# Kernel optimization log

Measured on AMD Instinct MI355X. Metric: run time of the kernel, lower is better.

The kernel has to match this reference:

```python
import jax, jax.numpy as jnp
import numpy as np

D_MODEL, N_HEADS, D_FF = 768, 12, 3072
B, S = 2, 2048
EPS = 1e-6

def _ln(x, alpha, bias):
    # Matches torch: std with Bessel correction (unbiased), scalar alpha/bias
    mean = x.mean(axis=-1, keepdims=True)
    std = jnp.std(x, axis=-1, keepdims=True, ddof=1)
    return alpha * (x - mean) / (std + EPS) + bias

def setup_inputs() -> dict:
    key = jax.random.key(0)
    ks = jax.random.split(key, 12)
    def w(k, shp):
        return jax.random.normal(k, shp, dtype=jnp.float32) * 0.02
    inp = {
        "x": jax.random.normal(ks[0], (B, S, D_MODEL), dtype=jnp.float32),
        "mask": jnp.ones((B, 1, 1, S), dtype=jnp.int32),
        "wq": w(ks[1], (D_MODEL, D_MODEL)), "bq": jnp.zeros((D_MODEL,), jnp.float32),
        "wk": w(ks[2], (D_MODEL, D_MODEL)), "bk": jnp.zeros((D_MODEL,), jnp.float32),
        "wv": w(ks[3], (D_MODEL, D_MODEL)), "bv": jnp.zeros((D_MODEL,), jnp.float32),
        "wo": w(ks[4], (D_MODEL, D_MODEL)), "bo": jnp.zeros((D_MODEL,), jnp.float32),
        "w1": w(ks[5], (D_MODEL, D_FF)), "b1": jnp.zeros((D_FF,), jnp.float32),
        "w2": w(ks[6], (D_FF, D_MODEL)), "b2": jnp.zeros((D_MODEL,), jnp.float32),
        "ln1_a": jnp.ones((1,), jnp.float32), "ln1_b": jnp.zeros((1,), jnp.float32),
        "ln2_a": jnp.ones((1,), jnp.float32), "ln2_b": jnp.zeros((1,), jnp.float32),
    }
    return inp

def reference(x, mask, wq, bq, wk, bk, wv, bv, wo, bo, w1, b1, w2, b2,
              ln1_a, ln1_b, ln2_a, ln2_b):
    d_k = D_MODEL // N_HEADS
    # --- residual 1: pre-LN self-attention ---
    h = _ln(x, ln1_a, ln1_b)
    q = (h @ wq + bq).reshape(B, S, N_HEADS, d_k).transpose(0, 2, 1, 3)
    k = (h @ wk + bk).reshape(B, S, N_HEADS, d_k).transpose(0, 2, 1, 3)
    v = (h @ wv + bv).reshape(B, S, N_HEADS, d_k).transpose(0, 2, 1, 3)
    scores = jnp.einsum('bhqd,bhkd->bhqk', q, k) / jnp.sqrt(jnp.float32(d_k))
    scores = jnp.where(mask == 0, jnp.float32(-1e9), scores)
    attn = jax.nn.softmax(scores, axis=-1)            # [B,H,S,S] materialized, as in source
    ctx = jnp.einsum('bhqk,bhkd->bhqd', attn, v)
    ctx = ctx.transpose(0, 2, 1, 3).reshape(B, S, D_MODEL)
    x = x + (ctx @ wo + bo)
    # --- residual 2: pre-LN FFN ---
    h = _ln(x, ln2_a, ln2_b)
    ffn = jax.nn.relu(h @ w1 + b1) @ w2 + b2
    return x + ffn
```

## Files before the change

kernel.cpp:

```cpp
#include <hip/hip_runtime.h>
#include <math.h>

#define DM    768
#define NH    12
#define DKH   64
#define DFF   3072
#define BATCH 2
#define SLEN  2048
#define MTOT  4096
#define LNEPS 1e-6f
#define QSCALE 0.18033688011112042f

typedef unsigned short u16;
typedef __attribute__((ext_vector_type(8))) short bf16x8;
typedef __attribute__((ext_vector_type(4))) float f32x4;
typedef __attribute__((ext_vector_type(4))) unsigned short us4;

__device__ __forceinline__ u16 f2bf(float f) {
    union { float f; unsigned int u; } v; v.f = f;
    unsigned int r = v.u + 0x7FFFu + ((v.u >> 16) & 1u);
    return (u16)(r >> 16);
}

__device__ __forceinline__ unsigned pk2bf_t(float lo, float hi) {
    union { float f; unsigned u; } a, b;
    a.f = lo; b.f = hi;
    return __builtin_amdgcn_perm(b.u, a.u, 0x07060302u);
}

__device__ __forceinline__ void gld16(const void* g, void* lds) {
    __builtin_amdgcn_global_load_lds(
        (const __attribute__((address_space(1))) unsigned int*)(unsigned long long)g,
        (__attribute__((address_space(3))) unsigned int*)(unsigned int)(unsigned long long)lds,
        16, 0, 0);
}

__device__ __forceinline__ void xcd_map(int id, int Nb, int& bm, int& bn) {
    int xcd = id & 7, loc = id >> 3;
    bn = loc % Nb;
    bm = (loc / Nb) * 8 + xcd;
}

__device__ __forceinline__ void ln_body(const float* __restrict__ x,
                                        u16* __restrict__ out,
                                        const float* __restrict__ alpha_p,
                                        const float* __restrict__ beta_p,
                                        const float* __restrict__ b2,
                                        float* __restrict__ out2, int row) {
    const float* xr = x + (size_t)row * DM;
    int t = threadIdx.x;
    float v0 = xr[t], v1 = xr[t + 256], v2 = xr[t + 512];
    float s = v0 + v1 + v2;
    #pragma unroll
    for (int off = 32; off > 0; off >>= 1) s += __shfl_down(s, off);
    __shared__ float red[4], red2[4];
    int wv = t >> 6, ln = t & 63;
    if (ln == 0) red[wv] = s;
    __syncthreads();
    float mean = (red[0] + red[1] + red[2] + red[3]) * (1.0f / 768.0f);
    float d0 = v0 - mean, d1 = v1 - mean, d2 = v2 - mean;
    float sq = d0 * d0 + d1 * d1 + d2 * d2;
    #pragma unroll
    for (int off = 32; off > 0; off >>= 1) sq += __shfl_down(sq, off);
    if (ln == 0) red2[wv] = sq;
    __syncthreads();
    float var = (red2[0] + red2[1] + red2[2] + red2[3]) * (1.0f / 767.0f);
    float scale = alpha_p[0] / (sqrtf(var) + LNEPS);
    float bias = beta_p[0];
    u16* orow = out + (size_t)row * DM;
    orow[t]       = f2bf(d0 * scale + bias);
    orow[t + 256] = f2bf(d1 * scale + bias);
    orow[t + 512] = f2bf(d2 * scale + bias);
    if (out2) {
        float* o2 = out2 + (size_t)row * DM;
        o2[t]       = v0 + b2[t];
        o2[t + 256] = v1 + b2[t + 256];
        o2[t + 512] = v2 + b2[t + 512];
    }
}

__global__ __launch_bounds__(256) void ln_kernel(const float* __restrict__ x,
                                                 u16* __restrict__ out,
                                                 const float* __restrict__ alpha_p,
                                                 const float* __restrict__ beta_p,
                                                 const float* __restrict__ b2,
                                                 float* __restrict__ out2) {
    ln_body(x, out, alpha_p, beta_p, b2, out2, blockIdx.x);
}

__device__ __forceinline__ void wcast_body(const float* __restrict__ src,
                                           u16* __restrict__ dst,
                                           int R, int C, int bx, int by) {
    __shared__ float tile[32][33];
    int t = threadIdx.x, tx = t & 31, ty = t >> 5;
    int r0 = by * 32, c0 = bx * 32;
    #pragma unroll
    for (int p = 0; p < 4; p++)
        tile[ty + p * 8][tx] = src[(size_t)(r0 + ty + p * 8) * C + c0 + tx];
    __syncthreads();
    #pragma unroll
    for (int p = 0; p < 4; p++)
        dst[(size_t)(c0 + ty + p * 8) * R + r0 + tx] = f2bf(tile[tx][ty + p * 8]);
}

__global__ __launch_bounds__(256) void prep_kernel(
        const float* __restrict__ x, u16* __restrict__ h,
        const float* __restrict__ ln1a, const float* __restrict__ ln1b,
        const float* __restrict__ wq, const float* __restrict__ wk,
        const float* __restrict__ wv, const float* __restrict__ wo,
        const float* __restrict__ w1, const float* __restrict__ w2,
        u16* __restrict__ wqT, u16* __restrict__ wkT, u16* __restrict__ wvT,
        u16* __restrict__ woT, u16* __restrict__ w1T, u16* __restrict__ w2T) {
    int bid = blockIdx.x;
    if (bid < MTOT) {
        ln_body(x, h, ln1a, ln1b, nullptr, nullptr, bid);
        return;
    }
    bid -= MTOT;
    const float* src; u16* dst; int R, C, bx, by;
    if (bid < 2304) {
        int j = bid / 576, tix = bid % 576;
        R = 768; C = 768; bx = tix % 24; by = tix / 24;
        src = (j == 0) ? wq : (j == 1) ? wk : (j == 2) ? wv : wo;
        dst = (j == 0) ? wqT : (j == 1) ? wkT : (j == 2) ? wvT : woT;
    } else if (bid < 4608) {
        int tix = bid - 2304;
        R = 768; C = 3072; bx = tix % 96; by = tix / 96;
        src = w1; dst = w1T;
    } else {
        int tix = bid - 4608;
        R = 3072; C = 768; bx = tix % 24; by = tix / 24;
        src = w2; dst = w2T;
    }
    wcast_body(src, dst, R, C, bx, by);
}

template<int EPI>
__device__ __forceinline__ void gemm128_core(const u16* __restrict__ A,
                                             const u16* __restrict__ Wt,
                                             const float* __restrict__ bias,
                                             const float* __restrict__ resid,
                                             void* __restrict__ Cout,
                                             int M, int N, int Kstride, int Kloop,
                                             float scale, int bm, int bn) {
    __shared__ __align__(16) u16 As[2][128 * 32];
    __shared__ __align__(16) u16 Bs[2][128 * 32];
    int t = threadIdx.x;
    int ln = t & 63, w = t >> 6;
    int wm = w >> 1, wn = w & 1;
    int quad = ln >> 4, col = ln & 15;
    int m0 = bm * 128, n0 = bn * 128;

    f32x4 acc[4][4];
    const f32x4 zero = {0.f, 0.f, 0.f, 0.f};
    #pragma unroll
    for (int i = 0; i < 4; i++)
        #pragma unroll
        for (int j = 0; j < 4; j++) acc[i][j] = zero;

    int st_ch = (((ln & 3) ^ ((ln >> 3) & 3))) * 8;
    const u16* Ag = A  + (size_t)(m0 + 32 * w + (ln >> 2)) * Kstride + st_ch;
    const u16* Bg = Wt + (size_t)(n0 + 32 * w + (ln >> 2)) * Kstride + st_ch;

    gld16(Ag,                As[0] + w * 1024);
    gld16(Ag + 16 * Kstride, As[0] + w * 1024 + 512);
    gld16(Bg,                Bs[0] + w * 1024);
    gld16(Bg + 16 * Kstride, Bs[0] + w * 1024 + 512);
    __syncthreads();

    int rch = (quad ^ ((col >> 1) & 3)) * 8;

    for (int k0 = 0; k0 < Kloop; k0 += 32) {
        int cur = (k0 >> 5) & 1, nxt = cur ^ 1;
        if (k0 + 32 < Kloop) {
            gld16(Ag + k0 + 32,                As[nxt] + w * 1024);
            gld16(Ag + k0 + 32 + 16 * Kstride, As[nxt] + w * 1024 + 512);
            gld16(Bg + k0 + 32,                Bs[nxt] + w * 1024);
            gld16(Bg + k0 + 32 + 16 * Kstride, Bs[nxt] + w * 1024 + 512);
        }
        bf16x8 af[4], bfr[4];
        #pragma unroll
        for (int i = 0; i < 4; i++)
            af[i] = *(const bf16x8*)&As[cur][(wm * 64 + i * 16 + col) * 32 + rch];
        #pragma unroll
        for (int j = 0; j < 4; j++)
            bfr[j] = *(const bf16x8*)&Bs[cur][(wn * 64 + j * 16 + col) * 32 + rch];
        #pragma unroll
        for (int i = 0; i < 4; i++)
            #pragma unroll
            for (int j = 0; j < 4; j++)
                acc[i][j] = __builtin_amdgcn_mfma_f32_16x16x32_bf16(af[i], bfr[j], acc[i][j], 0, 0, 0);
        __syncthreads();
    }

    #pragma unroll
    for (int i = 0; i < 4; i++) {
        int mb = m0 + wm * 64 + i * 16 + quad * 4;
        #pragma unroll
        for (int j = 0; j < 4; j++) {
            int n = n0 + wn * 64 + j * 16 + col;
            if (EPI == 0 || EPI == 1) {
                float bs = bias[n];
                u16* Cb = (u16*)Cout;
                #pragma unroll
                for (int r = 0; r < 4; r++) {
                    float f = (acc[i][j][r] + bs) * ((EPI == 0) ? scale : 1.0f);
                    if (EPI == 1) f = fmaxf(f, 0.f);
                    Cb[(size_t)(mb + r) * N + n] = f2bf(f);
                }
            } else if (EPI == 2) {
                float bs = bias[n];
                float* Cf = (float*)Cout;
                #pragma unroll
                for (int r = 0; r < 4; r++)
                    Cf[(size_t)(mb + r) * N + n] =
                        acc[i][j][r] + bs + resid[(size_t)(mb + r) * N + n];
            } else if (EPI == 3) {
                float bs = bias[n];
                u16* Cb = (u16*)Cout;
                us4 pk;
                #pragma unroll
                for (int r = 0; r < 4; r++) pk[r] = f2bf(acc[i][j][r] + bs);
                *(us4*)&Cb[(size_t)n * M + mb] = pk;
            } else {
                float* Cf = (float*)Cout;
                #pragma unroll
                for (int r = 0; r < 4; r++)
                    atomicAdd(&Cf[(size_t)(mb + r) * N + n], acc[i][j][r]);
            }
        }
    }
}

template<int EPI>
__global__ __launch_bounds__(256) void gemm_kernel(const u16* __restrict__ A,
                                                   const u16* __restrict__ Wt,
                                                   const float* __restrict__ bias,
                                                   const float* __restrict__ resid,
                                                   void* __restrict__ C,
                                                   int M, int N, int Kstride, int Kloop,
                                                   float scale, int Nb) {
    const u16* Az = A  + (size_t)blockIdx.z * Kloop;
    const u16* Wz = Wt + (size_t)blockIdx.z * Kloop;
    int bm, bn;
    xcd_map(blockIdx.x, Nb, bm, bn);
    gemm128_core<EPI>(Az, Wz, bias, resid, C, M, N, Kstride, Kloop, scale, bm, bn);
}

__global__ __launch_bounds__(256) void qkv_kernel(const u16* __restrict__ h,
        const u16* __restrict__ wqT, const u16* __restrict__ wkT, const u16* __restrict__ wvT,
        const float* __restrict__ bq, const float* __restrict__ bk, const float* __restrict__ bv,
        u16* __restrict__ q, u16* __restrict__ k, u16* __restrict__ vT) {
    int z = blockIdx.z;
    int bm, bn;
    xcd_map(blockIdx.x, 6, bm, bn);
    if (z == 0)      gemm128_core<0>(h, wqT, bq, nullptr, q,  MTOT, DM, DM, DM, QSCALE, bm, bn);
    else if (z == 1) gemm128_core<0>(h, wkT, bk, nullptr, k,  MTOT, DM, DM, DM, 1.0f,   bm, bn);
    else             gemm128_core<3>(h, wvT, bv, nullptr, vT, MTOT, DM, DM, DM, 1.0f,   bm, bn);
}

template<int EPI>
__global__ __launch_bounds__(256) void gemm64_kernel(const u16* __restrict__ A,
                                                     const u16* __restrict__ Wt,
                                                     const float* __restrict__ bias,
                                                     const float* __restrict__ resid,
                                                     void* __restrict__ Cout,
                                                     int M, int N, int Kstride, int Kloop,
                                                     int Nb) {
    __shared__ __align__(16) u16 As[2][64 * 32];
    __shared__ __align__(16) u16 Bs[2][64 * 32];
    int t = threadIdx.x, ln = t & 63, w = t >> 6;
    int wm = w >> 1, wn = w & 1;
    int quad = ln >> 4, col = ln & 15;
    int bm, bn;
    xcd_map(blockIdx.x, Nb, bm, bn);
    int m0 = bm * 64, n0 = bn * 64;

    f32x4 acc[2][2];
    const f32x4 zero = {0.f, 0.f, 0.f, 0.f};
    #pragma unroll
    for (int i = 0; i < 2; i++)
        #pragma unroll
        for (int j = 0; j < 2; j++) acc[i][j] = zero;

    int st_ch = (((ln & 3) ^ ((ln >> 3) & 3))) * 8;
    const u16* Ag = A  + (size_t)(m0 + 16 * w + (ln >> 2)) * Kstride + st_ch;
    const u16* Bg = Wt + (size_t)(n0 + 16 * w + (ln >> 2)) * Kstride + st_ch;
    gld16(Ag, As[0] + w * 512);
    gld16(Bg, Bs[0] + w * 512);
    __syncthreads();

    int rch = (quad ^ ((col >> 1) & 3)) * 8;

    for (int k0 = 0; k0 < Kloop; k0 += 32) {
        int cur = (k0 >> 5) & 1, nxt = cur ^ 1;
        if (k0 + 32 < Kloop) {
            gld16(Ag + k0 + 32, As[nxt] + w * 512);
            gld16(Bg + k0 + 32, Bs[nxt] + w * 512);
        }
        bf16x8 af[2], bfr[2];
        #pragma unroll
        for (int i = 0; i < 2; i++)
            af[i] = *(const bf16x8*)&As[cur][(wm * 32 + i * 16 + col) * 32 + rch];
        #pragma unroll
        for (int j = 0; j < 2; j++)
            bfr[j] = *(const bf16x8*)&Bs[cur][(wn * 32 + j * 16 + col) * 32 + rch];
        #pragma unroll
        for (int i = 0; i < 2; i++)
            #pragma unroll
            for (int j = 0; j < 2; j++)
                acc[i][j] = __builtin_amdgcn_mfma_f32_16x16x32_bf16(af[i], bfr[j], acc[i][j], 0, 0, 0);
        __syncthreads();
    }

    #pragma unroll
    for (int i = 0; i < 2; i++) {
        int mb = m0 + wm * 32 + i * 16 + quad * 4;
        #pragma unroll
        for (int j = 0; j < 2; j++) {
            int n = n0 + wn * 32 + j * 16 + col;
            float bs = bias[n];
            float* Cf = (float*)Cout;
            #pragma unroll
            for (int r = 0; r < 4; r++)
                Cf[(size_t)(mb + r) * N + n] =
                    acc[i][j][r] + bs + resid[(size_t)(mb + r) * N + n];
        }
    }
}

__global__ __launch_bounds__(256) void attn_kernel(const u16* __restrict__ qg,
                                                   const u16* __restrict__ kg,
                                                   const u16* __restrict__ vTg,
                                                   const int* __restrict__ mask,
                                                   u16* __restrict__ ctx) {
    __shared__ __align__(16) u16 Qs[64 * 64];
    __shared__ __align__(16) u16 KV[4][64 * 64];
    __shared__ __align__(16) u16 Ps[4][32 * 40];
    __shared__ __align__(16) float Msf[2][64];
    __shared__ float Lp[64];
    int t = threadIdx.x, ln = t & 63, w = t >> 6;
    int quad = ln >> 4, col = ln & 15;
    int qh = w >> 1, kh = w & 1;
    int bh = blockIdx.x, qb = blockIdx.y;
    int b = bh / NH, h = bh - b * NH;
    int q0 = qb * 64;
    size_t qkbase = ((size_t)b * SLEN) * DM + h * DKH;
    size_t vbase  = ((size_t)h * DKH) * MTOT + (size_t)b * SLEN;

    int sw_st = (((ln & 7) ^ (ln >> 3)) * 8);

    {
        const u16* g0 = qg + qkbase + (size_t)(q0 + 16 * w + (ln >> 3)) * DM + sw_st;
        gld16(g0,          Qs + w * 1024);
        gld16(g0 + 8 * DM, Qs + w * 1024 + 512);
        const u16* kg0 = kg + qkbase + (size_t)(16 * w + (ln >> 3)) * DM + sw_st;
        gld16(kg0,          KV[0] + w * 1024);
        gld16(kg0 + 8 * DM, KV[0] + w * 1024 + 512);
        const u16* vg0 = vTg + vbase + (size_t)(16 * w + (ln >> 3)) * MTOT + sw_st;
        gld16(vg0,            KV[2] + w * 1024);
        gld16(vg0 + 8 * MTOT, KV[2] + w * 1024 + 512);
        if (t < 64) Msf[0][t] = mask[b * SLEN + t] ? 0.f : -1e9f;
    }
    __syncthreads();

    bf16x8 bqf[2][2];
    #pragma unroll
    for (int qgi = 0; qgi < 2; qgi++) {
        int rq = qh * 32 + qgi * 16 + col;
        int cq = ((quad ^ (rq & 7)) * 8);
        bqf[qgi][0] = *(const bf16x8*)&Qs[rq * 64 + cq];
        bqf[qgi][1] = *(const bf16x8*)&Qs[rq * 64 + (cq ^ 32)];
    }

    bf16x8 vones;
    #pragma unroll
    for (int i = 0; i < 8; i++) vones[i] = (short)0x3F80;

    const u16* kpn = kg + qkbase + (size_t)(64 + 16 * w + (ln >> 3)) * DM + sw_st;
    const u16* vpn = vTg + vbase + (size_t)(16 * w + (ln >> 3)) * MTOT + 64 + sw_st;
    const int* mpn = mask + b * SLEN + 64 + t;

    f32x4 Ov[2][4], Lv[2];
    const f32x4 zero = {0.f, 0.f, 0.f, 0.f};
    #pragma unroll
    for (int qgi = 0; qgi < 2; qgi++) {
        Lv[qgi] = zero;
        #pragma unroll
        for (int dg = 0; dg < 4; dg++) Ov[qgi][dg] = zero;
    }
    u16* Psw = &Ps[w][0];

    for (int j0 = 0; j0 < SLEN; j0 += 64) {
        int cur = (j0 >> 6) & 1, nxt = cur ^ 1;
        if (j0 + 64 < SLEN) {
            gld16(kpn,            KV[nxt] + w * 1024);
            gld16(kpn + 8 * DM,   KV[nxt] + w * 1024 + 512);
            gld16(vpn,            KV[2 + nxt] + w * 1024);
            gld16(vpn + 8 * MTOT, KV[2 + nxt] + w * 1024 + 512);
            if (t < 64) Msf[nxt][t] = *mpn ? 0.f : -1e9f;
            kpn += 64 * DM; vpn += 64; mpn += 64;
        }

        bf16x8 ak[2][2];
        #pragma unroll
        for (int kgi = 0; kgi < 2; kgi++) {
            int rk = kh * 32 + kgi * 16 + col;
            int ck = ((quad ^ (rk & 7)) * 8);
            ak[kgi][0] = *(const bf16x8*)&KV[cur][rk * 64 + ck];
            ak[kgi][1] = *(const bf16x8*)&KV[cur][rk * 64 + (ck ^ 32)];
        }
        #pragma unroll
        for (int kgi = 0; kgi < 2; kgi++) {
            f32x4 bias4 = *(const f32x4*)&Msf[cur][kh * 32 + kgi * 16 + quad * 4];
            #pragma unroll
            for (int qgi = 0; qgi < 2; qgi++) {
                f32x4 S = __builtin_amdgcn_mfma_f32_16x16x32_bf16(ak[kgi][0], bqf[qgi][0], bias4, 0, 0, 0);
                S       = __builtin_amdgcn_mfma_f32_16x16x32_bf16(ak[kgi][1], bqf[qgi][1], S,     0, 0, 0);
                float p0 = exp2f(S[0]), p1 = exp2f(S[1]);
                float p2 = exp2f(S[2]), p3 = exp2f(S[3]);
                uint2 pk;
                pk.x = pk2bf_t(p0, p1);
                pk.y = pk2bf_t(p2, p3);
                *(uint2*)&Psw[(qgi * 16 + col) * 40 + kgi * 16 + quad * 4] = pk;
            }
        }
        bf16x8 ap[2];
        #pragma unroll
        for (int qgi = 0; qgi < 2; qgi++) {
            ap[qgi] = *(const bf16x8*)&Psw[(qgi * 16 + col) * 40 + quad * 8];
            Lv[qgi] = __builtin_amdgcn_mfma_f32_16x16x32_bf16(ap[qgi], vones, Lv[qgi], 0, 0, 0);
        }
        #pragma unroll
        for (int dg = 0; dg < 4; dg++) {
            int rv = dg * 16 + col;
            int cv = (((kh * 4 + quad) ^ (rv & 7)) * 8);
            bf16x8 bv = *(const bf16x8*)&KV[2 + cur][rv * 64 + cv];
            Ov[0][dg] = __builtin_amdgcn_mfma_f32_16x16x32_bf16(ap[0], bv, Ov[0][dg], 0, 0, 0);
            Ov[1][dg] = __builtin_amdgcn_mfma_f32_16x16x32_bf16(ap[1], bv, Ov[1][dg], 0, 0, 0);
        }
        __syncthreads();
    }

    float* Osh = (float*)&KV[0][0];
    if (kh == 1) {
        #pragma unroll
        for (int qgi = 0; qgi < 2; qgi++) {
            #pragma unroll
            for (int dg = 0; dg < 4; dg++)
                *(f32x4*)&Osh[(qh * 64 + dg * 16 + col) * 36 + qgi * 16 + quad * 4] = Ov[qgi][dg];
            if (col == 0) {
                #pragma unroll
                for (int r = 0; r < 4; r++)
                    Lp[qh * 32 + qgi * 16 + quad * 4 + r] = Lv[qgi][r];
            }
        }
    }
    __syncthreads();
    if (kh == 0) {
        #pragma unroll
        for (int qgi = 0; qgi < 2; qgi++) {
            float linv[4];
            #pragma unroll
            for (int r = 0; r < 4; r++) {
                int ql = qh * 32 + qgi * 16 + quad * 4 + r;
                linv[r] = 1.0f / (Lv[qgi][r] + Lp[ql]);
            }
            #pragma unroll
            for (int dg = 0; dg < 4; dg++) {
                f32x4 oo = *(const f32x4*)&Osh[(qh * 64 + dg * 16 + col) * 36 + qgi * 16 + quad * 4];
                #pragma unroll
                for (int r = 0; r < 4; r++) {
                    int qrow = q0 + qh * 32 + qgi * 16 + quad * 4 + r;
                    ctx[qkbase + (size_t)qrow * DM + dg * 16 + col] =
                        f2bf((Ov[qgi][dg][r] + oo[r]) * linv[r]);
                }
            }
        }
    }
}

extern "C" void kernel_launch(void* const* d_in, const int* in_sizes, int n_in,
                              void* d_out, int out_size, void* d_ws, size_t ws_size,
                              hipStream_t stream) {
    const float* x    = (const float*)d_in[0];
    const int*   mask = (const int*)d_in[1];
    const float* wq   = (const float*)d_in[2];
    const float* bq   = (const float*)d_in[3];
    const float* wk   = (const float*)d_in[4];
    const float* bk   = (const float*)d_in[5];
    const float* wv   = (const float*)d_in[6];
    const float* bv   = (const float*)d_in[7];
    const float* wo   = (const float*)d_in[8];
    const float* bo   = (const float*)d_in[9];
    const float* w1   = (const float*)d_in[10];
    const float* b1   = (const float*)d_in[11];
    const float* w2   = (const float*)d_in[12];
    const float* b2   = (const float*)d_in[13];
    const float* ln1a = (const float*)d_in[14];
    const float* ln1b = (const float*)d_in[15];
    const float* ln2a = (const float*)d_in[16];
    const float* ln2b = (const float*)d_in[17];
    float* out = (float*)d_out;

    char* w8 = (char*)d_ws;
    u16*   ffn = (u16*)(w8 + 0);
    u16*   q   = (u16*)(w8 + 0);
    u16*   kb  = (u16*)(w8 + 6291456);
    u16*   vT  = (u16*)(w8 + 12582912);
    u16*   ctx = (u16*)(w8 + 18874368);
    u16*   h   = (u16*)(w8 + 25165824);
    float* x1  = (float*)(w8 + 31457280);
    u16*   wqT = (u16*)(w8 + 44040192);
    u16*   wkT = (u16*)(w8 + 45219840);
    u16*   wvT = (u16*)(w8 + 46399488);
    u16*   woT = (u16*)(w8 + 47579136);
    u16*   w1T = (u16*)(w8 + 48758784);
    u16*   w2T = (u16*)(w8 + 53477376);

    prep_kernel<<<MTOT + 6912, 256, 0, stream>>>(x, h, ln1a, ln1b,
                                                 wq, wk, wv, wo, w1, w2,
                                                 wqT, wkT, wvT, woT, w1T, w2T);
    qkv_kernel<<<dim3(192, 1, 3), 256, 0, stream>>>(h, wqT, wkT, wvT, bq, bk, bv, q, kb, vT);
    attn_kernel<<<dim3(BATCH * NH, SLEN / 64), 256, 0, stream>>>(q, kb, vT, mask, ctx);
    gemm64_kernel<2><<<768, 256, 0, stream>>>(ctx, woT, bo, x, (void*)x1,
                                              MTOT, DM, DM, DM, 12);
    ln_kernel<<<MTOT, 256, 0, stream>>>(x1, h, ln2a, ln2b, b2, out);
    gemm_kernel<1><<<768, 256, 0, stream>>>(h, w1T, b1, nullptr, (void*)ffn,
                                            MTOT, DFF, DM, DM, 1.0f, 24);
    gemm_kernel<5><<<dim3(192, 1, 2), 256, 0, stream>>>(ffn, w2T, nullptr, nullptr, (void*)out,
                                                        MTOT, DM, DFF, DFF / 2, 1.0f, 6);
}
```

Before: 285.7 us.

## Keep softmax probabilities in registers for PV MFMA, drop LDS round-trip

The attention kernel used to write exp'd scores to a per-wave LDS buffer and read them back as MFMA A operands. Now it feeds the probabilities straight from registers into 16x16x16 bf16 MFMAs, computing the transposed output O^T = V^T P^T and the row sums with a ones vector. This removes LDS stores and loads and the buffer itself. The epilogue is also restructured to normalize in LDS and then write ctx with vectorized bf16 stores, with an extra barrier. The trade-off is twice as many MFMA instructions at half the K depth, plus one more sync in the epilogue.

```diff
diff --git a/kernel.cpp b/kernel.cpp
--- a/kernel.cpp
+++ b/kernel.cpp
@@ -13,6 +13,7 @@
 
 typedef unsigned short u16;
 typedef __attribute__((ext_vector_type(8))) short bf16x8;
+typedef __attribute__((ext_vector_type(4))) short bf16x4;
 typedef __attribute__((ext_vector_type(4))) float f32x4;
 typedef __attribute__((ext_vector_type(4))) unsigned short us4;
 
@@ -336,7 +337,6 @@
                                                    u16* __restrict__ ctx) {
     __shared__ __align__(16) u16 Qs[64 * 64];
     __shared__ __align__(16) u16 KV[4][64 * 64];
-    __shared__ __align__(16) u16 Ps[4][32 * 40];
     __shared__ __align__(16) float Msf[2][64];
     __shared__ float Lp[64];
     int t = threadIdx.x, ln = t & 63, w = t >> 6;
@@ -373,23 +373,22 @@
         bqf[qgi][1] = *(const bf16x8*)&Qs[rq * 64 + (cq ^ 32)];
     }
 
-    bf16x8 vones;
-    #pragma unroll
-    for (int i = 0; i < 8; i++) vones[i] = (short)0x3F80;
+    bf16x4 aones;
+    #pragma unroll
+    for (int i = 0; i < 4; i++) aones[i] = (short)0x3F80;
 
     const u16* kpn = kg + qkbase + (size_t)(64 + 16 * w + (ln >> 3)) * DM + sw_st;
     const u16* vpn = vTg + vbase + (size_t)(16 * w + (ln >> 3)) * MTOT + 64 + sw_st;
     const int* mpn = mask + b * SLEN + 64 + t;
 
-    f32x4 Ov[2][4], Lv[2];
+    f32x4 Ot[2][4], Lv[2];
     const f32x4 zero = {0.f, 0.f, 0.f, 0.f};
     #pragma unroll
     for (int qgi = 0; qgi < 2; qgi++) {
         Lv[qgi] = zero;
         #pragma unroll
-        for (int dg = 0; dg < 4; dg++) Ov[qgi][dg] = zero;
-    }
-    u16* Psw = &Ps[w][0];
+        for (int dg = 0; dg < 4; dg++) Ot[qgi][dg] = zero;
+    }
 
     for (int j0 = 0; j0 < SLEN; j0 += 64) {
         int cur = (j0 >> 6) & 1, nxt = cur ^ 1;
@@ -410,6 +409,7 @@
             ak[kgi][0] = *(const bf16x8*)&KV[cur][rk * 64 + ck];
             ak[kgi][1] = *(const bf16x8*)&KV[cur][rk * 64 + (ck ^ 32)];
         }
+        bf16x4 Pb[2][2];
         #pragma unroll
         for (int kgi = 0; kgi < 2; kgi++) {
             f32x4 bias4 = *(const f32x4*)&Msf[cur][kh * 32 + kgi * 16 + quad * 4];
@@ -417,27 +417,24 @@
             for (int qgi = 0; qgi < 2; qgi++) {
                 f32x4 S = __builtin_amdgcn_mfma_f32_16x16x32_bf16(ak[kgi][0], bqf[qgi][0], bias4, 0, 0, 0);
                 S       = __builtin_amdgcn_mfma_f32_16x16x32_bf16(ak[kgi][1], bqf[qgi][1], S,     0, 0, 0);
-                float p0 = exp2f(S[0]), p1 = exp2f(S[1]);
-                float p2 = exp2f(S[2]), p3 = exp2f(S[3]);
-                uint2 pk;
-                pk.x = pk2bf_t(p0, p1);
-                pk.y = pk2bf_t(p2, p3);
-                *(uint2*)&Psw[(qgi * 16 + col) * 40 + kgi * 16 + quad * 4] = pk;
+                union { uint2 u; bf16x4 h4; } pk;
+                pk.u.x = pk2bf_t(exp2f(S[0]), exp2f(S[1]));
+                pk.u.y = pk2bf_t(exp2f(S[2]), exp2f(S[3]));
+                Pb[kgi][qgi] = pk.h4;
+                Lv[qgi] = __builtin_amdgcn_mfma_f32_16x16x16bf16_1k(aones, pk.h4, Lv[qgi], 0, 0, 0);
             }
         }
-        bf16x8 ap[2];
-        #pragma unroll
-        for (int qgi = 0; qgi < 2; qgi++) {
-            ap[qgi] = *(const bf16x8*)&Psw[(qgi * 16 + col) * 40 + quad * 8];
-            Lv[qgi] = __builtin_amdgcn_mfma_f32_16x16x32_bf16(ap[qgi], vones, Lv[qgi], 0, 0, 0);
-        }
-        #pragma unroll
-        for (int dg = 0; dg < 4; dg++) {
-            int rv = dg * 16 + col;
-            int cv = (((kh * 4 + quad) ^ (rv & 7)) * 8);
-            bf16x8 bv = *(const bf16x8*)&KV[2 + cur][rv * 64 + cv];
-            Ov[0][dg] = __builtin_amdgcn_mfma_f32_16x16x32_bf16(ap[0], bv, Ov[0][dg], 0, 0, 0);
-            Ov[1][dg] = __builtin_amdgcn_mfma_f32_16x16x32_bf16(ap[1], bv, Ov[1][dg], 0, 0, 0);
+        #pragma unroll
+        for (int kgi = 0; kgi < 2; kgi++) {
+            int sc = kh * 4 + kgi * 2 + (quad >> 1);
+            #pragma unroll
+            for (int dg = 0; dg < 4; dg++) {
+                int row = dg * 16 + col;
+                int off = ((sc ^ (row & 7)) * 8 + (quad & 1) * 4);
+                bf16x4 av = *(const bf16x4*)&KV[2 + cur][row * 64 + off];
+                Ot[0][dg] = __builtin_amdgcn_mfma_f32_16x16x16bf16_1k(av, Pb[kgi][0], Ot[0][dg], 0, 0, 0);
+                Ot[1][dg] = __builtin_amdgcn_mfma_f32_16x16x16bf16_1k(av, Pb[kgi][1], Ot[1][dg], 0, 0, 0);
+            }
         }
         __syncthreads();
     }
@@ -448,34 +445,37 @@
         for (int qgi = 0; qgi < 2; qgi++) {
             #pragma unroll
             for (int dg = 0; dg < 4; dg++)
-                *(f32x4*)&Osh[(qh * 64 + dg * 16 + col) * 36 + qgi * 16 + quad * 4] = Ov[qgi][dg];
-            if (col == 0) {
+                *(f32x4*)&Osh[(qh * 32 + qgi * 16 + col) * 68 + dg * 16 + quad * 4] = Ot[qgi][dg];
+            if (quad == 0) Lp[qh * 32 + qgi * 16 + col] = Lv[qgi][0];
+        }
+    }
+    __syncthreads();
+    if (kh == 0) {
+        #pragma unroll
+        for (int qgi = 0; qgi < 2; qgi++) {
+            float linv = 1.0f / (Lv[qgi][0] + Lp[qh * 32 + qgi * 16 + col]);
+            #pragma unroll
+            for (int dg = 0; dg < 4; dg++) {
+                float* p = &Osh[(qh * 32 + qgi * 16 + col) * 68 + dg * 16 + quad * 4];
+                f32x4 oo = *(const f32x4*)p;
                 #pragma unroll
-                for (int r = 0; r < 4; r++)
-                    Lp[qh * 32 + qgi * 16 + quad * 4 + r] = Lv[qgi][r];
+                for (int r = 0; r < 4; r++) oo[r] = (oo[r] + Ot[qgi][dg][r]) * linv;
+                *(f32x4*)p = oo;
             }
         }
     }
     __syncthreads();
-    if (kh == 0) {
-        #pragma unroll
-        for (int qgi = 0; qgi < 2; qgi++) {
-            float linv[4];
-            #pragma unroll
-            for (int r = 0; r < 4; r++) {
-                int ql = qh * 32 + qgi * 16 + quad * 4 + r;
-                linv[r] = 1.0f / (Lv[qgi][r] + Lp[ql]);
-            }
-            #pragma unroll
-            for (int dg = 0; dg < 4; dg++) {
-                f32x4 oo = *(const f32x4*)&Osh[(qh * 64 + dg * 16 + col) * 36 + qgi * 16 + quad * 4];
-                #pragma unroll
-                for (int r = 0; r < 4; r++) {
-                    int qrow = q0 + qh * 32 + qgi * 16 + quad * 4 + r;
-                    ctx[qkbase + (size_t)qrow * DM + dg * 16 + col] =
-                        f2bf((Ov[qgi][dg][r] + oo[r]) * linv[r]);
-                }
-            }
+    {
+        int qrow = q0 + (t >> 2);
+        const float* src = &Osh[(t >> 2) * 68 + (t & 3) * 16];
+        u16* dst = ctx + qkbase + (size_t)qrow * DM + (t & 3) * 16;
+        #pragma unroll
+        for (int i = 0; i < 4; i++) {
+            f32x4 v = *(const f32x4*)&src[i * 4];
+            uint2 pk;
+            pk.x = pk2bf_t(v[0], v[1]);
+            pk.y = pk2bf_t(v[2], v[3]);
+            *(uint2*)&dst[i * 4] = pk;
         }
     }
 }
```

Result: no change. 288.4 us (+0.9%).
